# Kernel tuning notes

Measured on AMD Instinct MI355X. Metric: run time of the kernel, lower is better.

## Reference

```python
import jax, jax.numpy as jnp
import numpy as np

D_INNER = 8192
DT_RANK = 8
D_STATE = 16

def silu(v):
    return v * jax.nn.sigmoid(v)

def setup_inputs() -> dict:
    key = jax.random.key(0)
    ks = jax.random.split(key, 12)
    s = 0.02  # weight scale to keep activations sane
    return {
        "x": jax.random.normal(ks[0], (4096,), jnp.float32),
        "ssm_state": jax.random.normal(ks[1], (D_INNER, D_STATE), jnp.float32) * 0.1,
        "conv_buffer": jnp.zeros((D_INNER, 3), jnp.float32),
        "W_in": jax.random.normal(ks[2], (2 * D_INNER, 4096), jnp.float32) * s,
        "conv_w": jax.random.normal(ks[3], (D_INNER, 4), jnp.float32) * 0.5,
        "conv_b": jax.random.normal(ks[4], (D_INNER,), jnp.float32) * 0.1,
        "W_xp": jax.random.normal(ks[5], (DT_RANK + 2 * D_STATE, D_INNER), jnp.float32) * s,
        "W_dt": jax.random.normal(ks[6], (D_INNER, DT_RANK), jnp.float32) * s,
        "b_dt": jax.random.normal(ks[7], (D_INNER,), jnp.float32) * 0.1,
        "A_log": jax.random.uniform(ks[8], (D_INNER, D_STATE), jnp.float32),
        "D_param": jnp.ones((D_INNER,), jnp.float32),
        "W_out": jax.random.normal(ks[9], (4096, D_INNER), jnp.float32) * s,
    }

def reference(x, ssm_state, conv_buffer, W_in, conv_w, conv_b, W_xp, W_dt, b_dt, A_log, D_param, W_out):
    # in_proj: (2*d_inner,)
    xz = W_in @ x
    x_branch, z = xz[:D_INNER], xz[D_INNER:]
    # buffer shift (note: original appends x_branch to buffer AND again to conv_in)
    new_buf = jnp.concatenate([conv_buffer[:, 1:], x_branch[:, None]], axis=1)  # (d_inner, d_conv-1)
    conv_in = jnp.concatenate([new_buf, x_branch[:, None]], axis=1)             # (d_inner, d_conv)
    x_conv = silu(jnp.sum(conv_in * conv_w, axis=-1) + conv_b)                  # (d_inner,)
    # selective scan step
    xp = W_xp @ x_conv                                                          # (dt_rank + 2*d_state,)
    dt = jax.nn.softplus(W_dt @ xp[:DT_RANK] + b_dt)                            # (d_inner,)
    B = xp[DT_RANK:DT_RANK + D_STATE]
    C = xp[DT_RANK + D_STATE:]
    A = -jnp.exp(A_log)                                                         # (d_inner, d_state)
    A_bar = jnp.exp(dt[:, None] * A)
    new_h = A_bar * ssm_state + (dt[:, None] * B[None, :]) * x_conv[:, None]
    y = jnp.sum(new_h * C[None, :], axis=-1) + D_param * x_conv
    y = y * silu(z)
    out = W_out @ y
    return out, new_h
```

## Files before the change

kernel.cpp:

```cpp
#include <hip/hip_runtime.h>
#include <hip/hip_bf16.h>
#include <math.h>

#define D_INNER 8192
#define D_MODEL 4096
#define DT_RANK 8
#define D_STATE 16

__global__ __launch_bounds__(256) void gemv_in_kernel(
    const float* __restrict__ W_in, const float* __restrict__ x,
    const float* __restrict__ conv_buffer, const float* __restrict__ conv_w,
    const float* __restrict__ conv_b,
    float* __restrict__ x_conv, float* __restrict__ silu_z) {
  const int wave = threadIdx.x >> 6;
  const int lane = threadIdx.x & 63;
  const int row = blockIdx.x * 4 + wave;
  const float4* __restrict__ Wr = (const float4*)(W_in + (size_t)row * D_MODEL);
  const float4* __restrict__ x4 = (const float4*)x;

  float acc = 0.f;
#pragma unroll 8
  for (int it = 0; it < 16; ++it) {
    float4 w = Wr[lane + it * 64];
    float4 v = x4[lane + it * 64];
    acc += w.x * v.x + w.y * v.y + w.z * v.z + w.w * v.w;
  }
#pragma unroll
  for (int off = 32; off; off >>= 1) acc += __shfl_down(acc, off, 64);

  if (lane == 0) {
    if (row < D_INNER) {
      float pre = conv_buffer[row * 3 + 1] * conv_w[row * 4 + 0]
                + conv_buffer[row * 3 + 2] * conv_w[row * 4 + 1]
                + acc * (conv_w[row * 4 + 2] + conv_w[row * 4 + 3])
                + conv_b[row];
      x_conv[row] = pre / (1.f + __expf(-pre));
    } else {
      const int i = row - D_INNER;
      silu_z[i] = acc / (1.f + __expf(-acc));
    }
  }
}

__global__ __launch_bounds__(256) void gemv_xp_kernel(
    const float* __restrict__ W_xp, const float* __restrict__ x_conv,
    float* __restrict__ xp) {
  const int j = blockIdx.x;
  const float4* __restrict__ Wr = (const float4*)(W_xp + (size_t)j * D_INNER);
  const float4* __restrict__ xc4 = (const float4*)x_conv;

  float acc = 0.f;
#pragma unroll
  for (int it = 0; it < 8; ++it) {
    float4 w = Wr[threadIdx.x + it * 256];
    float4 v = xc4[threadIdx.x + it * 256];
    acc += w.x * v.x + w.y * v.y + w.z * v.z + w.w * v.w;
  }
#pragma unroll
  for (int off = 32; off; off >>= 1) acc += __shfl_down(acc, off, 64);

  __shared__ float part[4];
  if ((threadIdx.x & 63) == 0) part[threadIdx.x >> 6] = acc;
  __syncthreads();
  if (threadIdx.x == 0) xp[j] = part[0] + part[1] + part[2] + part[3];
}

__global__ __launch_bounds__(256) void cell_kernel(
    const float* __restrict__ W_dt, const float* __restrict__ b_dt,
    const float* __restrict__ A_log, const float* __restrict__ ssm_state,
    const float* __restrict__ D_param, const float* __restrict__ x_conv,
    const float* __restrict__ silu_z, const float* __restrict__ xp,
    float* __restrict__ new_h, float* __restrict__ y) {
  const int i = blockIdx.x * blockDim.x + threadIdx.x;
  if (i >= D_INNER) return;

  float d = b_dt[i];
#pragma unroll
  for (int j = 0; j < DT_RANK; ++j) d += W_dt[i * DT_RANK + j] * xp[j];
  const float dt = (d > 20.f) ? d : log1pf(__expf(d));

  const float xc = x_conv[i];
  float y_acc = 0.f;
#pragma unroll
  for (int s = 0; s < D_STATE; ++s) {
    const float A    = -__expf(A_log[i * D_STATE + s]);
    const float Abar = __expf(dt * A);
    const float h    = Abar * ssm_state[i * D_STATE + s]
                     + dt * xp[DT_RANK + s] * xc;
    new_h[i * D_STATE + s] = h;
    y_acc += h * xp[DT_RANK + D_STATE + s];
  }
  y_acc += D_param[i] * xc;
  y[i] = y_acc * silu_z[i];
}

__global__ __launch_bounds__(256) void gemv_out_kernel(
    const float* __restrict__ W_out, const float* __restrict__ y,
    float* __restrict__ out) {
  const int wave = threadIdx.x >> 6;
  const int lane = threadIdx.x & 63;
  const int row = blockIdx.x * 4 + wave;
  const float4* __restrict__ Wr = (const float4*)(W_out + (size_t)row * D_INNER);
  const float4* __restrict__ y4 = (const float4*)y;

  float acc = 0.f;
#pragma unroll 8
  for (int it = 0; it < 32; ++it) {
    float4 w = Wr[lane + it * 64];
    float4 v = y4[lane + it * 64];
    acc += w.x * v.x + w.y * v.y + w.z * v.z + w.w * v.w;
  }
#pragma unroll
  for (int off = 32; off; off >>= 1) acc += __shfl_down(acc, off, 64);
  if (lane == 0) out[row] = acc;
}

extern "C" void kernel_launch(void* const* d_in, const int* in_sizes, int n_in,
                              void* d_out, int out_size, void* d_ws, size_t ws_size,
                              hipStream_t stream) {
  const float* x           = (const float*)d_in[0];
  const float* ssm_state   = (const float*)d_in[1];
  const float* conv_buffer = (const float*)d_in[2];
  const float* W_in        = (const float*)d_in[3];
  const float* conv_w      = (const float*)d_in[4];
  const float* conv_b      = (const float*)d_in[5];
  const float* W_xp        = (const float*)d_in[6];
  const float* W_dt        = (const float*)d_in[7];
  const float* b_dt        = (const float*)d_in[8];
  const float* A_log       = (const float*)d_in[9];
  const float* D_param     = (const float*)d_in[10];
  const float* W_out       = (const float*)d_in[11];

  float* out   = (float*)d_out;
  float* new_h = (float*)d_out + D_MODEL;

  float* ws     = (float*)d_ws;
  float* x_conv = ws;
  float* silu_z = ws + 8192;
  float* xp     = ws + 16384;
  float* y      = ws + 16448;

  gemv_in_kernel<<<(2 * D_INNER) / 4, 256, 0, stream>>>(
      W_in, x, conv_buffer, conv_w, conv_b, x_conv, silu_z);
  gemv_xp_kernel<<<DT_RANK + 2 * D_STATE, 256, 0, stream>>>(W_xp, x_conv, xp);
  cell_kernel<<<D_INNER / 256, 256, 0, stream>>>(
      W_dt, b_dt, A_log, ssm_state, D_param, x_conv, silu_z, xp, new_h, y);
  gemv_out_kernel<<<D_MODEL / 4, 256, 0, stream>>>(W_out, y, out);
}
```

Baseline: 453.0 us.

## Split xp GEMV across blocks, widen cell kernel, use nontemporal weight loads

```diff
diff --git a/kernel.cpp b/kernel.cpp
--- a/kernel.cpp
+++ b/kernel.cpp
@@ -1,11 +1,16 @@
 #include <hip/hip_runtime.h>
-#include <hip/hip_bf16.h>
 #include <math.h>
 
 #define D_INNER 8192
 #define D_MODEL 4096
 #define DT_RANK 8
 #define D_STATE 16
+
+typedef float f32x4 __attribute__((ext_vector_type(4)));
+
+__device__ __forceinline__ float dot4(f32x4 a, f32x4 b) {
+  return a.x * b.x + a.y * b.y + a.z * b.z + a.w * b.w;
+}
 
 __global__ __launch_bounds__(256) void gemv_in_kernel(
     const float* __restrict__ W_in, const float* __restrict__ x,
@@ -15,15 +20,15 @@
   const int wave = threadIdx.x >> 6;
   const int lane = threadIdx.x & 63;
   const int row = blockIdx.x * 4 + wave;
-  const float4* __restrict__ Wr = (const float4*)(W_in + (size_t)row * D_MODEL);
-  const float4* __restrict__ x4 = (const float4*)x;
+  const f32x4* __restrict__ Wr = (const f32x4*)(W_in + (size_t)row * D_MODEL);
+  const f32x4* __restrict__ x4 = (const f32x4*)x;
 
   float acc = 0.f;
 #pragma unroll 8
   for (int it = 0; it < 16; ++it) {
-    float4 w = Wr[lane + it * 64];
-    float4 v = x4[lane + it * 64];
-    acc += w.x * v.x + w.y * v.y + w.z * v.z + w.w * v.w;
+    f32x4 w = __builtin_nontemporal_load(&Wr[lane + it * 64]);
+    f32x4 v = x4[lane + it * 64];
+    acc += dot4(w, v);
   }
 #pragma unroll
   for (int off = 32; off; off >>= 1) acc += __shfl_down(acc, off, 64);
@@ -44,54 +49,66 @@
 
 __global__ __launch_bounds__(256) void gemv_xp_kernel(
     const float* __restrict__ W_xp, const float* __restrict__ x_conv,
-    float* __restrict__ xp) {
-  const int j = blockIdx.x;
-  const float4* __restrict__ Wr = (const float4*)(W_xp + (size_t)j * D_INNER);
-  const float4* __restrict__ xc4 = (const float4*)x_conv;
+    float* __restrict__ xp_part) {
+  const int j = blockIdx.x >> 3;
+  const int c = blockIdx.x & 7;
+  const f32x4* __restrict__ Wr  = (const f32x4*)(W_xp + (size_t)j * D_INNER + c * 1024);
+  const f32x4* __restrict__ xc4 = (const f32x4*)(x_conv + c * 1024);
 
-  float acc = 0.f;
-#pragma unroll
-  for (int it = 0; it < 8; ++it) {
-    float4 w = Wr[threadIdx.x + it * 256];
-    float4 v = xc4[threadIdx.x + it * 256];
-    acc += w.x * v.x + w.y * v.y + w.z * v.z + w.w * v.w;
-  }
+  float acc = dot4(Wr[threadIdx.x], xc4[threadIdx.x]);
 #pragma unroll
   for (int off = 32; off; off >>= 1) acc += __shfl_down(acc, off, 64);
 
   __shared__ float part[4];
   if ((threadIdx.x & 63) == 0) part[threadIdx.x >> 6] = acc;
   __syncthreads();
-  if (threadIdx.x == 0) xp[j] = part[0] + part[1] + part[2] + part[3];
+  if (threadIdx.x == 0) xp_part[blockIdx.x] = part[0] + part[1] + part[2] + part[3];
 }
 
 __global__ __launch_bounds__(256) void cell_kernel(
     const float* __restrict__ W_dt, const float* __restrict__ b_dt,
     const float* __restrict__ A_log, const float* __restrict__ ssm_state,
     const float* __restrict__ D_param, const float* __restrict__ x_conv,
-    const float* __restrict__ silu_z, const float* __restrict__ xp,
+    const float* __restrict__ silu_z, const float* __restrict__ xp_part,
     float* __restrict__ new_h, float* __restrict__ y) {
-  const int i = blockIdx.x * blockDim.x + threadIdx.x;
-  if (i >= D_INNER) return;
+  __shared__ float xp_s[DT_RANK + 2 * D_STATE];
+  if (threadIdx.x < DT_RANK + 2 * D_STATE) {
+    float s = 0.f;
+#pragma unroll
+    for (int c = 0; c < 8; ++c) s += xp_part[threadIdx.x * 8 + c];
+    xp_s[threadIdx.x] = s;
+  }
+  __syncthreads();
 
-  float d = b_dt[i];
-#pragma unroll
-  for (int j = 0; j < DT_RANK; ++j) d += W_dt[i * DT_RANK + j] * xp[j];
+  const int t  = blockIdx.x * 256 + threadIdx.x;
+  const int i  = t >> 2;
+  const int sq = (t & 3) << 2;
+
+  const f32x4 wd0 = *(const f32x4*)(W_dt + i * DT_RANK);
+  const f32x4 wd1 = *(const f32x4*)(W_dt + i * DT_RANK + 4);
+  float d = b_dt[i]
+          + wd0.x * xp_s[0] + wd0.y * xp_s[1] + wd0.z * xp_s[2] + wd0.w * xp_s[3]
+          + wd1.x * xp_s[4] + wd1.y * xp_s[5] + wd1.z * xp_s[6] + wd1.w * xp_s[7];
   const float dt = (d > 20.f) ? d : log1pf(__expf(d));
+  const float xc = x_conv[i];
 
-  const float xc = x_conv[i];
+  const f32x4 al = *(const f32x4*)(A_log + i * D_STATE + sq);
+  const f32x4 h0 = *(const f32x4*)(ssm_state + i * D_STATE + sq);
+  f32x4 h;
   float y_acc = 0.f;
 #pragma unroll
-  for (int s = 0; s < D_STATE; ++s) {
-    const float A    = -__expf(A_log[i * D_STATE + s]);
+  for (int s = 0; s < 4; ++s) {
+    const float A    = -__expf(al[s]);
     const float Abar = __expf(dt * A);
-    const float h    = Abar * ssm_state[i * D_STATE + s]
-                     + dt * xp[DT_RANK + s] * xc;
-    new_h[i * D_STATE + s] = h;
-    y_acc += h * xp[DT_RANK + D_STATE + s];
+    const float hv   = Abar * h0[s] + dt * xp_s[DT_RANK + sq + s] * xc;
+    h[s] = hv;
+    y_acc += hv * xp_s[DT_RANK + D_STATE + sq + s];
   }
-  y_acc += D_param[i] * xc;
-  y[i] = y_acc * silu_z[i];
+  *(f32x4*)(new_h + i * D_STATE + sq) = h;
+
+  y_acc += __shfl_down(y_acc, 1, 64);
+  y_acc += __shfl_down(y_acc, 2, 64);
+  if ((t & 3) == 0) y[i] = (y_acc + D_param[i] * xc) * silu_z[i];
 }
 
 __global__ __launch_bounds__(256) void gemv_out_kernel(
@@ -100,15 +117,15 @@
   const int wave = threadIdx.x >> 6;
   const int lane = threadIdx.x & 63;
   const int row = blockIdx.x * 4 + wave;
-  const float4* __restrict__ Wr = (const float4*)(W_out + (size_t)row * D_INNER);
-  const float4* __restrict__ y4 = (const float4*)y;
+  const f32x4* __restrict__ Wr = (const f32x4*)(W_out + (size_t)row * D_INNER);
+  const f32x4* __restrict__ y4 = (const f32x4*)y;
 
   float acc = 0.f;
 #pragma unroll 8
   for (int it = 0; it < 32; ++it) {
-    float4 w = Wr[lane + it * 64];
-    float4 v = y4[lane + it * 64];
-    acc += w.x * v.x + w.y * v.y + w.z * v.z + w.w * v.w;
+    f32x4 w = __builtin_nontemporal_load(&Wr[lane + it * 64]);
+    f32x4 v = y4[lane + it * 64];
+    acc += dot4(w, v);
   }
 #pragma unroll
   for (int off = 32; off; off >>= 1) acc += __shfl_down(acc, off, 64);
@@ -134,16 +151,17 @@
   float* out   = (float*)d_out;
   float* new_h = (float*)d_out + D_MODEL;
 
-  float* ws     = (float*)d_ws;
-  float* x_conv = ws;
-  float* silu_z = ws + 8192;
-  float* xp     = ws + 16384;
-  float* y      = ws + 16448;
+  float* ws      = (float*)d_ws;
+  float* x_conv  = ws;
+  float* silu_z  = ws + 8192;
+  float* xp_part = ws + 16384;
+  float* y       = ws + 16704;
 
   gemv_in_kernel<<<(2 * D_INNER) / 4, 256, 0, stream>>>(
       W_in, x, conv_buffer, conv_w, conv_b, x_conv, silu_z);
-  gemv_xp_kernel<<<DT_RANK + 2 * D_STATE, 256, 0, stream>>>(W_xp, x_conv, xp);
-  cell_kernel<<<D_INNER / 256, 256, 0, stream>>>(
-      W_dt, b_dt, A_log, ssm_state, D_param, x_conv, silu_z, xp, new_h, y);
+  gemv_xp_kernel<<<(DT_RANK + 2 * D_STATE) * 8, 256, 0, stream>>>(
+      W_xp, x_conv, xp_part);
+  cell_kernel<<<(D_INNER * 4) / 256, 256, 0, stream>>>(
+      W_dt, b_dt, A_log, ssm_state, D_param, x_conv, silu_z, xp_part, new_h, y);
   gemv_out_kernel<<<D_MODEL / 4, 256, 0, stream>>>(W_out, y, out);
 }
```

Measured after the change: 432.4 us. 1.05x faster.
